# Performance work log

Hardware: AMD Instinct MI355X
Metric: run time of the kernel (lower is better)

The kernel has to match this reference:

```python
import jax, jax.numpy as jnp
import numpy as np

D_MODEL = 1024
N_HEADS = 16
HEAD_DIM = D_MODEL // N_HEADS


def setup_inputs() -> dict:
    key = jax.random.key(0)
    k_x, k_wqkv, k_bqkv, k_wp, k_bp = jax.random.split(key, 5)
    B, N = 2, 2048
    x = jax.random.normal(k_x, (B, N, D_MODEL), dtype=jnp.float32)
    s = 1.0 / np.sqrt(D_MODEL)
    w_qkv = jax.random.uniform(k_wqkv, (D_MODEL, 3 * D_MODEL), jnp.float32, -s, s)
    b_qkv = jax.random.uniform(k_bqkv, (3 * D_MODEL,), jnp.float32, -s, s)
    w_proj = jax.random.uniform(k_wp, (D_MODEL, D_MODEL), jnp.float32, -s, s)
    b_proj = jax.random.uniform(k_bp, (D_MODEL,), jnp.float32, -s, s)
    return {"x": x, "w_qkv": w_qkv, "b_qkv": b_qkv, "w_proj": w_proj, "b_proj": b_proj}


def reference(x, w_qkv, b_qkv, w_proj, b_proj):
    B, N, C = x.shape
    scale = HEAD_DIM ** (-0.5)
    qkv = x @ w_qkv + b_qkv  # [B, N, 3C]
    qkv = qkv.reshape(B, N, 3, N_HEADS, HEAD_DIM).transpose(2, 0, 3, 1, 4)
    q, k, v = qkv[0], qkv[1], qkv[2]  # each [B, H, N, Dh]
    p = jnp.einsum('bhnd,bhmd->bhnm', q, k) * scale  # [B, H, N, N]
    p = jax.nn.softmax(p, axis=-1)
    o = jnp.einsum('bhnm,bhmd->bhnd', p, v)  # [B, H, N, Dh]
    o = o.transpose(0, 2, 1, 3).reshape(B, N, C)
    return o @ w_proj + b_proj
```

## Files before the change

kernel.cpp:

```cpp
#include <hip/hip_runtime.h>


typedef short v8s __attribute__((ext_vector_type(8)));
typedef float v4f __attribute__((ext_vector_type(4)));
typedef unsigned int v4u __attribute__((ext_vector_type(4)));

#define QSCALE 0.18033688011112042f

#if defined(__has_builtin)
# if __has_builtin(__builtin_amdgcn_exp2f)
#  define EXP2(x) __builtin_amdgcn_exp2f(x)
# endif
#endif
#ifndef EXP2
static __device__ __forceinline__ float exp2_asm(float x) {
    float r;
    asm volatile("v_exp_f32 %0, %1\n\ts_nop 1" : "=v"(r) : "v"(x));
    return r;
}
# define EXP2(x) exp2_asm(x)
#endif

static __device__ __forceinline__ unsigned short f2bf_fast(float f) {
    union { float f; unsigned int u; } a;
    a.f = f;
    return (unsigned short)((a.u + 0x8000u) >> 16);
}

static __device__ __forceinline__ unsigned int pack_bf16(float lo, float hi) {
    union { float f; unsigned int u; } a, b;
    a.f = lo; b.f = hi;
    return __builtin_amdgcn_perm(b.u + 0x8000u, a.u + 0x8000u, 0x07060302u);
}

#define GLD16(g, l) __builtin_amdgcn_global_load_lds( \
    (const __attribute__((address_space(1))) unsigned int*)(g), \
    (__attribute__((address_space(3))) unsigned int*)(l), 16, 0, 0)

__global__ __launch_bounds__(256) void prep(const float* __restrict__ x,
                                            unsigned short* __restrict__ xb,
                                            const float* __restrict__ w_qkv,
                                            unsigned short* __restrict__ wqkvt,
                                            const float* __restrict__ w_proj,
                                            unsigned short* __restrict__ wprojt) {
    __shared__ float tile[32][33];
    const int bid = blockIdx.x, tid = threadIdx.x;
    if (bid < 4096) {
        int i = bid * 256 + tid;
        float4 f = ((const float4*)x)[i];
        ushort4 o;
        o.x = f2bf_fast(f.x); o.y = f2bf_fast(f.y); o.z = f2bf_fast(f.z); o.w = f2bf_fast(f.w);
        ((ushort4*)xb)[i] = o;
        return;
    }
    const float* w; unsigned short* wt; int R, C, bx, by;
    if (bid < 7168) { w = w_qkv; wt = wqkvt; R = 1024; C = 3072;
                      int t = bid - 4096; bx = t % 96; by = t / 96; }
    else            { w = w_proj; wt = wprojt; R = 1024; C = 1024;
                      int t = bid - 7168; bx = t & 31; by = t >> 5; }
    const int tx = tid & 31, ty = tid >> 5;
    const int c0 = bx * 32, r0 = by * 32;
#pragma unroll
    for (int j = 0; j < 32; j += 8)
        tile[ty + j][tx] = w[(r0 + ty + j) * C + c0 + tx];
    __syncthreads();
#pragma unroll
    for (int j = 0; j < 32; j += 8)
        wt[(c0 + ty + j) * R + r0 + tx] = f2bf_fast(tile[tx][ty + j]);
}

__global__ __launch_bounds__(256) void gemm_bt(const unsigned short* __restrict__ A,
                                               const unsigned short* __restrict__ Bt,
                                               const float* __restrict__ bias,
                                               int M, int N, int K, int mode,
                                               unsigned short* __restrict__ qo,
                                               unsigned short* __restrict__ ko,
                                               unsigned short* __restrict__ vto,
                                               float* __restrict__ outp) {
    __shared__ unsigned short Sh[24576];
    const int tid = threadIdx.x;
    const int wave = tid >> 6, lane = tid & 63;
    const int quad = lane >> 4, l16 = lane & 15;
    const int W = gridDim.x;
    const int id = blockIdx.y * W + blockIdx.x;
    const int s = (id & 7) * (W << 2) + (id >> 3);
    const int bm = (s / W) * 128, bn = (s % W) * 128;
    const int wm = (wave >> 1) * 64, wn = (wave & 1) * 64;
    const int rsw = (quad ^ ((l16 >> 1) & 3)) << 3;

    v4f acc[4][4];
#pragma unroll
    for (int i = 0; i < 4; i++)
#pragma unroll
        for (int j = 0; j < 4; j++) acc[i][j] = (v4f){0.f, 0.f, 0.f, 0.f};

#define GSTAGE(off, kk) do { \
    _Pragma("unroll") \
    for (int i_ = 0; i_ < 2; i_++) { \
        int c_ = i_ * 256 + tid; \
        int r_ = c_ >> 2; \
        int g_ = ((c_ & 3) ^ ((r_ >> 1) & 3)) << 3; \
        GLD16(&A[(bm + r_) * K + (kk) + g_], &Sh[(off) + (c_ << 3)]); \
        GLD16(&Bt[(bn + r_) * K + (kk) + g_], &Sh[(off) + 4096 + (c_ << 3)]); \
    } } while (0)

#define GCOMP(off) do { \
    v8s af_[4], bf_[4]; \
    _Pragma("unroll") \
    for (int mi_ = 0; mi_ < 4; mi_++) \
        af_[mi_] = *(const v8s*)&Sh[(off) + (wm + mi_ * 16 + l16) * 32 + rsw]; \
    _Pragma("unroll") \
    for (int ni_ = 0; ni_ < 4; ni_++) \
        bf_[ni_] = *(const v8s*)&Sh[(off) + 4096 + (wn + ni_ * 16 + l16) * 32 + rsw]; \
    _Pragma("unroll") \
    for (int mi_ = 0; mi_ < 4; mi_++) \
        _Pragma("unroll") \
        for (int ni_ = 0; ni_ < 4; ni_++) \
            acc[mi_][ni_] = __builtin_amdgcn_mfma_f32_16x16x32_bf16( \
                af_[mi_], bf_[ni_], acc[mi_][ni_], 0, 0, 0); \
    } while (0)

    const int nt = K >> 5;
    int o0 = 0, o1 = 8192, o2 = 16384;
    GSTAGE(o0, 0);
    GSTAGE(o1, 32);
    for (int t = 0; t < nt - 1; ++t) {
        asm volatile("s_waitcnt vmcnt(4)" ::: "memory");
        __builtin_amdgcn_s_barrier();
        __builtin_amdgcn_sched_barrier(0);
        if (t + 2 < nt) GSTAGE(o2, (t + 2) << 5);
        GCOMP(o0);
        int tmp = o0; o0 = o1; o1 = o2; o2 = tmp;
    }
    asm volatile("s_waitcnt vmcnt(0)" ::: "memory");
    __builtin_amdgcn_s_barrier();
    __builtin_amdgcn_sched_barrier(0);
    GCOMP(o0);
#undef GSTAGE
#undef GCOMP

    if (mode == 1) {
#pragma unroll
        for (int mi = 0; mi < 4; mi++)
#pragma unroll
            for (int ni = 0; ni < 4; ni++) {
                int col = bn + wn + ni * 16 + l16;
                float bv = bias[col];
                int row0 = bm + wm + mi * 16 + quad * 4;
#pragma unroll
                for (int r = 0; r < 4; r++)
                    outp[(row0 + r) * N + col] = acc[mi][ni][r] + bv;
            }
    } else if (bn < 2048) {
        const int isq = (bn < 1024);
        unsigned short* dst = isq ? qo : ko;
        const float sc = isq ? QSCALE : 1.0f;
        __syncthreads();
#pragma unroll
        for (int mi = 0; mi < 4; mi++)
#pragma unroll
            for (int ni = 0; ni < 4; ni++) {
                int c = wn + ni * 16 + l16;
                float bv = bias[bn + c];
                int r0 = wm + mi * 16 + quad * 4;
#pragma unroll
                for (int r = 0; r < 4; r++)
                    Sh[(r0 + r) * 136 + c] = f2bf_fast((acc[mi][ni][r] + bv) * sc);
            }
        __syncthreads();
        const int bb = bm >> 11, nb = bm & 2047;
#pragma unroll
        for (int j = 0; j < 8; j++) {
            int idx = j * 256 + tid;
            int r = idx >> 4, c8 = idx & 15;
            int rem = (bn + c8 * 8) & 1023;
            int h = rem >> 6, dh = rem & 63;
            *(int4*)&dst[(((bb * 16 + h) << 11) + nb + r) * 64 + dh] =
                *(const int4*)&Sh[r * 136 + c8 * 8];
        }
    } else {
        __syncthreads();
#pragma unroll
        for (int mi = 0; mi < 4; mi++)
#pragma unroll
            for (int ni = 0; ni < 4; ni++) {
                int col = bn + wn + ni * 16 + l16;
                float bv = bias[col];
                ushort4 pk;
                pk.x = f2bf_fast(acc[mi][ni][0] + bv);
                pk.y = f2bf_fast(acc[mi][ni][1] + bv);
                pk.z = f2bf_fast(acc[mi][ni][2] + bv);
                pk.w = f2bf_fast(acc[mi][ni][3] + bv);
                *(ushort4*)&Sh[(wn + ni * 16 + l16) * 136 +
                               wm + ((mi >> 1) * 32) + quad * 8 + ((mi & 1) * 4)] = pk;
            }
        __syncthreads();
        const int b = bm >> 11, n_base = bm & 2047;
#pragma unroll
        for (int j = 0; j < 8; j++) {
            int idx = j * 256 + tid;
            int Lcol = idx >> 4, rc = idx & 15;
            int rem = (bn + Lcol) & 1023;
            int h = rem >> 6, dh = rem & 63;
            *(int4*)&vto[((((b * 16 + h) * 64 + dh) << 11) + n_base + rc * 8)] =
                *(const int4*)&Sh[Lcol * 136 + rc * 8];
        }
    }
}

__global__ __launch_bounds__(256, 4) void attn(const unsigned short* __restrict__ q,
                                               const unsigned short* __restrict__ k,
                                               const unsigned short* __restrict__ vt,
                                               unsigned short* __restrict__ o) {
    __shared__ unsigned short Ks[2][64 * 64];
    __shared__ unsigned short Vs[2][64 * 64];
    const int tid = threadIdx.x;
    const int wave = tid >> 6, lane = tid & 63;
    const int quad = lane >> 4, l16 = lane & 15;
    const int sw = l16 & 7;

    const int id = blockIdx.y * 32 + blockIdx.x;
    const int bh = (id & 7) * 4 + ((id >> 3) & 3);
    const int wq0 = (id >> 5) * 64 + wave * 16;
    const int rowg = bh * 2048 + wq0;

    v8s qf[2];
#pragma unroll
    for (int half = 0; half < 2; half++)
        qf[half] = *(const v8s*)&q[(rowg + l16) * 64 + half * 32 + quad * 8];

    v8s onef;
#pragma unroll
    for (int j = 0; j < 8; j++) onef[j] = (short)0x3F80;

    v4f oacc[4];
    v4f lacc = (v4f){0.f, 0.f, 0.f, 0.f};
#pragma unroll
    for (int dt = 0; dt < 4; dt++) oacc[dt] = (v4f){0.f, 0.f, 0.f, 0.f};

    const unsigned short* kbase = k + (((long)bh << 11) * 64);
    const unsigned short* vbase = vt + (((long)bh * 64) << 11);

#define STAGE(buf, n0s) do { \
    _Pragma("unroll") \
    for (int i_ = 0; i_ < 2; i_++) { \
        int c_ = i_ * 256 + tid; \
        int r_ = c_ >> 3; \
        int chs_ = ((c_ & 7) ^ (r_ & 7)) << 3; \
        GLD16(&kbase[((n0s) + r_) * 64 + chs_], &Ks[buf][c_ << 3]); \
        GLD16(&vbase[(r_ << 11) + (n0s) + chs_], &Vs[buf][c_ << 3]); \
    } } while (0)

    auto tile = [&](const unsigned short* Kc, const unsigned short* Vc) {
        v4f s[4];
        __builtin_amdgcn_s_setprio(1);
#pragma unroll
        for (int ni = 0; ni < 4; ni++) {
            int rowk = (ni * 16 + l16) * 64;
            v8s kf0 = *(const v8s*)&Kc[rowk + ((quad ^ sw) << 3)];
            v8s kf1 = *(const v8s*)&Kc[rowk + (((4 + quad) ^ sw) << 3)];
            v4f z = (v4f){0.f, 0.f, 0.f, 0.f};
            z = __builtin_amdgcn_mfma_f32_16x16x32_bf16(kf0, qf[0], z, 0, 0, 0);
            z = __builtin_amdgcn_mfma_f32_16x16x32_bf16(kf1, qf[1], z, 0, 0, 0);
            s[ni] = z;
        }
        __builtin_amdgcn_s_setprio(0);

        v8s af[2];
#pragma unroll
        for (int t = 0; t < 2; t++) {
            v4u w;
            w[0] = pack_bf16(EXP2(s[2 * t][0]),     EXP2(s[2 * t][1]));
            w[1] = pack_bf16(EXP2(s[2 * t][2]),     EXP2(s[2 * t][3]));
            w[2] = pack_bf16(EXP2(s[2 * t + 1][0]), EXP2(s[2 * t + 1][1]));
            w[3] = pack_bf16(EXP2(s[2 * t + 1][2]), EXP2(s[2 * t + 1][3]));
            union { v4u u; v8s s8; } cv;
            cv.u = w;
            af[t] = cv.s8;
        }

        __builtin_amdgcn_s_setprio(1);
#pragma unroll
        for (int dt = 0; dt < 4; dt++) {
            int rowv = (dt * 16 + l16) * 64;
            v8s vf0 = *(const v8s*)&Vc[rowv + ((quad ^ sw) << 3)];
            v8s vf1 = *(const v8s*)&Vc[rowv + (((4 + quad) ^ sw) << 3)];
            oacc[dt] = __builtin_amdgcn_mfma_f32_16x16x32_bf16(af[0], vf0, oacc[dt], 0, 0, 0);
            oacc[dt] = __builtin_amdgcn_mfma_f32_16x16x32_bf16(af[1], vf1, oacc[dt], 0, 0, 0);
        }
        lacc = __builtin_amdgcn_mfma_f32_16x16x32_bf16(af[0], onef, lacc, 0, 0, 0);
        lacc = __builtin_amdgcn_mfma_f32_16x16x32_bf16(af[1], onef, lacc, 0, 0, 0);
        __builtin_amdgcn_s_setprio(0);
    };

    STAGE(0, 0);
    for (int n0 = 0; n0 < 2048; n0 += 128) {
        __syncthreads();
        if (n0 + 64 < 2048) STAGE(1, n0 + 64);
        tile(Ks[0], Vs[0]);
        __syncthreads();
        if (n0 + 128 < 2048) STAGE(0, n0 + 128);
        tile(Ks[1], Vs[1]);
    }
#undef STAGE

    const int b = bh >> 4, h = bh & 15;
#pragma unroll
    for (int r = 0; r < 4; r++) {
        float linv = 1.0f / lacc[r];
        int n = wq0 + quad * 4 + r;
#pragma unroll
        for (int dt = 0; dt < 4; dt++)
            o[(b * 2048 + n) * 1024 + h * 64 + dt * 16 + l16] =
                f2bf_fast(oacc[dt][r] * linv);
    }
}

extern "C" void kernel_launch(void* const* d_in, const int* in_sizes, int n_in,
                              void* d_out, int out_size, void* d_ws, size_t ws_size,
                              hipStream_t stream) {
    const float* x      = (const float*)d_in[0];
    const float* w_qkv  = (const float*)d_in[1];
    const float* b_qkv  = (const float*)d_in[2];
    const float* w_proj = (const float*)d_in[3];
    const float* b_proj = (const float*)d_in[4];
    float* outp = (float*)d_out;

    unsigned short* ws     = (unsigned short*)d_ws;
    unsigned short* xb     = ws;
    unsigned short* wqkvt  = ws + 4194304;
    unsigned short* wprojt = wqkvt + 3145728;
    unsigned short* qws    = wprojt + 1048576;
    unsigned short* kws    = qws + 4194304;
    unsigned short* vtws   = kws + 4194304;
    unsigned short* ows    = xb;

    prep<<<8192, 256, 0, stream>>>(x, xb, w_qkv, wqkvt, w_proj, wprojt);
    gemm_bt<<<dim3(24, 32), 256, 0, stream>>>(xb, wqkvt, b_qkv, 4096, 3072, 1024, 0,
                                              qws, kws, vtws, nullptr);
    attn<<<dim3(32, 32), 256, 0, stream>>>(qws, kws, vtws, ows);
    gemm_bt<<<dim3(8, 32), 256, 0, stream>>>(ows, wprojt, b_proj, 4096, 1024, 1024, 1,
                                             nullptr, nullptr, nullptr, outp);
}
```

Before: 180.6 us.

## Process two 16-row query groups per wave in attention to reuse K/V tiles

Each attention wave now handles 32 query rows as two 16-row groups instead of 16 rows. Every K and V fragment read from shared memory feeds MFMAs for both groups, and each block stages K/V once for 128 query rows instead of 64. The grid is halved and launch bounds drop to 2 blocks per SM so the doubled accumulators and Q fragments fit in registers. This cuts shared-memory reads and global K/V traffic per query, at the cost of lower occupancy and fewer blocks to spread across the CUs.

```diff
diff --git a/kernel.cpp b/kernel.cpp
--- a/kernel.cpp
+++ b/kernel.cpp
@@ -208,7 +208,7 @@
     }
 }
 
-__global__ __launch_bounds__(256, 4) void attn(const unsigned short* __restrict__ q,
+__global__ __launch_bounds__(256, 2) void attn(const unsigned short* __restrict__ q,
                                                const unsigned short* __restrict__ k,
                                                const unsigned short* __restrict__ vt,
                                                unsigned short* __restrict__ o) {
@@ -219,24 +219,30 @@
     const int quad = lane >> 4, l16 = lane & 15;
     const int sw = l16 & 7;
 
-    const int id = blockIdx.y * 32 + blockIdx.x;
+    const int id = blockIdx.y * 16 + blockIdx.x;
     const int bh = (id & 7) * 4 + ((id >> 3) & 3);
-    const int wq0 = (id >> 5) * 64 + wave * 16;
+    const int wq0 = (id >> 5) * 128 + wave * 32;
     const int rowg = bh * 2048 + wq0;
 
-    v8s qf[2];
-#pragma unroll
-    for (int half = 0; half < 2; half++)
-        qf[half] = *(const v8s*)&q[(rowg + l16) * 64 + half * 32 + quad * 8];
+    v8s qf[2][2];
+#pragma unroll
+    for (int g = 0; g < 2; g++)
+#pragma unroll
+        for (int half = 0; half < 2; half++)
+            qf[g][half] = *(const v8s*)&q[(rowg + g * 16 + l16) * 64 + half * 32 + quad * 8];
 
     v8s onef;
 #pragma unroll
     for (int j = 0; j < 8; j++) onef[j] = (short)0x3F80;
 
-    v4f oacc[4];
-    v4f lacc = (v4f){0.f, 0.f, 0.f, 0.f};
-#pragma unroll
-    for (int dt = 0; dt < 4; dt++) oacc[dt] = (v4f){0.f, 0.f, 0.f, 0.f};
+    v4f oacc[2][4];
+    v4f lacc[2];
+#pragma unroll
+    for (int g = 0; g < 2; g++) {
+        lacc[g] = (v4f){0.f, 0.f, 0.f, 0.f};
+#pragma unroll
+        for (int dt = 0; dt < 4; dt++) oacc[g][dt] = (v4f){0.f, 0.f, 0.f, 0.f};
+    }
 
     const unsigned short* kbase = k + (((long)bh << 11) * 64);
     const unsigned short* vbase = vt + (((long)bh * 64) << 11);
@@ -252,32 +258,37 @@
     } } while (0)
 
     auto tile = [&](const unsigned short* Kc, const unsigned short* Vc) {
-        v4f s[4];
+        v4f s[2][4];
         __builtin_amdgcn_s_setprio(1);
 #pragma unroll
         for (int ni = 0; ni < 4; ni++) {
             int rowk = (ni * 16 + l16) * 64;
             v8s kf0 = *(const v8s*)&Kc[rowk + ((quad ^ sw) << 3)];
             v8s kf1 = *(const v8s*)&Kc[rowk + (((4 + quad) ^ sw) << 3)];
-            v4f z = (v4f){0.f, 0.f, 0.f, 0.f};
-            z = __builtin_amdgcn_mfma_f32_16x16x32_bf16(kf0, qf[0], z, 0, 0, 0);
-            z = __builtin_amdgcn_mfma_f32_16x16x32_bf16(kf1, qf[1], z, 0, 0, 0);
-            s[ni] = z;
+#pragma unroll
+            for (int g = 0; g < 2; g++) {
+                v4f z = (v4f){0.f, 0.f, 0.f, 0.f};
+                z = __builtin_amdgcn_mfma_f32_16x16x32_bf16(kf0, qf[g][0], z, 0, 0, 0);
+                z = __builtin_amdgcn_mfma_f32_16x16x32_bf16(kf1, qf[g][1], z, 0, 0, 0);
+                s[g][ni] = z;
+            }
         }
         __builtin_amdgcn_s_setprio(0);
 
-        v8s af[2];
-#pragma unroll
-        for (int t = 0; t < 2; t++) {
-            v4u w;
-            w[0] = pack_bf16(EXP2(s[2 * t][0]),     EXP2(s[2 * t][1]));
-            w[1] = pack_bf16(EXP2(s[2 * t][2]),     EXP2(s[2 * t][3]));
-            w[2] = pack_bf16(EXP2(s[2 * t + 1][0]), EXP2(s[2 * t + 1][1]));
-            w[3] = pack_bf16(EXP2(s[2 * t + 1][2]), EXP2(s[2 * t + 1][3]));
-            union { v4u u; v8s s8; } cv;
-            cv.u = w;
-            af[t] = cv.s8;
-        }
+        v8s af[2][2];
+#pragma unroll
+        for (int g = 0; g < 2; g++)
+#pragma unroll
+            for (int t = 0; t < 2; t++) {
+                v4u w;
+                w[0] = pack_bf16(EXP2(s[g][2 * t][0]),     EXP2(s[g][2 * t][1]));
+                w[1] = pack_bf16(EXP2(s[g][2 * t][2]),     EXP2(s[g][2 * t][3]));
+                w[2] = pack_bf16(EXP2(s[g][2 * t + 1][0]), EXP2(s[g][2 * t + 1][1]));
+                w[3] = pack_bf16(EXP2(s[g][2 * t + 1][2]), EXP2(s[g][2 * t + 1][3]));
+                union { v4u u; v8s s8; } cv;
+                cv.u = w;
+                af[g][t] = cv.s8;
+            }
 
         __builtin_amdgcn_s_setprio(1);
 #pragma unroll
@@ -285,11 +296,17 @@
             int rowv = (dt * 16 + l16) * 64;
             v8s vf0 = *(const v8s*)&Vc[rowv + ((quad ^ sw) << 3)];
             v8s vf1 = *(const v8s*)&Vc[rowv + (((4 + quad) ^ sw) << 3)];
-            oacc[dt] = __builtin_amdgcn_mfma_f32_16x16x32_bf16(af[0], vf0, oacc[dt], 0, 0, 0);
-            oacc[dt] = __builtin_amdgcn_mfma_f32_16x16x32_bf16(af[1], vf1, oacc[dt], 0, 0, 0);
-        }
-        lacc = __builtin_amdgcn_mfma_f32_16x16x32_bf16(af[0], onef, lacc, 0, 0, 0);
-        lacc = __builtin_amdgcn_mfma_f32_16x16x32_bf16(af[1], onef, lacc, 0, 0, 0);
+#pragma unroll
+            for (int g = 0; g < 2; g++) {
+                oacc[g][dt] = __builtin_amdgcn_mfma_f32_16x16x32_bf16(af[g][0], vf0, oacc[g][dt], 0, 0, 0);
+                oacc[g][dt] = __builtin_amdgcn_mfma_f32_16x16x32_bf16(af[g][1], vf1, oacc[g][dt], 0, 0, 0);
+            }
+        }
+#pragma unroll
+        for (int g = 0; g < 2; g++) {
+            lacc[g] = __builtin_amdgcn_mfma_f32_16x16x32_bf16(af[g][0], onef, lacc[g], 0, 0, 0);
+            lacc[g] = __builtin_amdgcn_mfma_f32_16x16x32_bf16(af[g][1], onef, lacc[g], 0, 0, 0);
+        }
         __builtin_amdgcn_s_setprio(0);
     };
 
@@ -306,14 +323,16 @@
 
     const int b = bh >> 4, h = bh & 15;
 #pragma unroll
-    for (int r = 0; r < 4; r++) {
-        float linv = 1.0f / lacc[r];
-        int n = wq0 + quad * 4 + r;
-#pragma unroll
-        for (int dt = 0; dt < 4; dt++)
-            o[(b * 2048 + n) * 1024 + h * 64 + dt * 16 + l16] =
-                f2bf_fast(oacc[dt][r] * linv);
-    }
+    for (int g = 0; g < 2; g++)
+#pragma unroll
+        for (int r = 0; r < 4; r++) {
+            float linv = 1.0f / lacc[g][r];
+            int n = wq0 + g * 16 + quad * 4 + r;
+#pragma unroll
+            for (int dt = 0; dt < 4; dt++)
+                o[(b * 2048 + n) * 1024 + h * 64 + dt * 16 + l16] =
+                    f2bf_fast(oacc[g][dt][r] * linv);
+        }
 }
 
 extern "C" void kernel_launch(void* const* d_in, const int* in_sizes, int n_in,
@@ -338,7 +357,7 @@
     prep<<<8192, 256, 0, stream>>>(x, xb, w_qkv, wqkvt, w_proj, wprojt);
     gemm_bt<<<dim3(24, 32), 256, 0, stream>>>(xb, wqkvt, b_qkv, 4096, 3072, 1024, 0,
                                               qws, kws, vtws, nullptr);
-    attn<<<dim3(32, 32), 256, 0, stream>>>(qws, kws, vtws, ows);
+    attn<<<dim3(16, 32), 256, 0, stream>>>(qws, kws, vtws, ows);
     gemm_bt<<<dim3(8, 32), 256, 0, stream>>>(ows, wprojt, b_proj, 4096, 1024, 1024, 1,
                                              nullptr, nullptr, nullptr, outp);
 }
```

Result: faster. 173.0 us (-4.3%).
